# Kernel optimization log

Hardware: AMD Instinct MI355X
Metric: run time of the kernel (lower is better)

## Reference

```python
import jax, jax.numpy as jnp
import numpy as np

SIGMA = 1.0   # noise std (unit-variance synthetic input)
P = 11        # patch size p1
K = 16        # number of similar patches k1
WIN = 65      # search window w (odd)
S = 3         # reference-patch stride
ALPHA = 0.5   # n2n alpha


def _unfold(x, ksize, stride):
    # (N,1,H,W) -> (N, ksize*ksize, Ho, Wo); kernel positions row-major (== torch F.unfold for C=1)
    return jax.lax.conv_general_dilated_patches(
        x, (ksize, ksize), (stride, stride), 'VALID',
        dimension_numbers=('NCHW', 'OIHW', 'NCHW'))


def block_matching(x, k, p, w, s):
    N, _, H, W = x.shape
    v = w // 2
    assert (H - p + 1) % s == 1 and (W - p + 1) % s == 1  # no edge-case branches needed
    Href = (H - p) // s + 1
    Wref = (W - p) // s + 1
    x_pad = jnp.pad(x, ((0, 0), (0, 0), (v, v), (v, v)))  # zero pad; invalid candidates masked below
    # |patch|^2 / p^2 at every position of the padded image (== F.avg_pool2d(x**2, p))
    sq = jax.lax.reduce_window(x_pad * x_pad, 0.0, jax.lax.add,
                               (1, 1, p, p), (1, 1, 1, 1), 'VALID') / (p * p)
    norms = _unfold(sq, 2 * v + 1, s)                                  # (N,(2v+1)^2,Href,Wref)
    norms = norms.reshape(N, 2 * v + 1, 2 * v + 1, Href, Wref).transpose(0, 3, 4, 1, 2)
    lw = _unfold(x_pad, 2 * v + p, s) / p                              # (N,(2v+p)^2,Href,Wref)
    lw = lw.reshape(N, 2 * v + p, 2 * v + p, Href, Wref).transpose(0, 3, 4, 1, 2)
    G = N * Href * Wref
    lw = lw.reshape(1, G, 2 * v + p, 2 * v + p)
    ref = lw[0, :, v:-v, v:-v][:, None]                                # (G,1,p,p) reference patches
    sp = jax.lax.conv_general_dilated(
        lw, ref, (1, 1), 'VALID',
        dimension_numbers=('NCHW', 'OIHW', 'NCHW'),
        feature_group_count=G)                                         # (1,G,2v+1,2v+1)
    dist = norms.reshape(1, G, 2 * v + 1, 2 * v + 1) - 2.0 * sp
    dist = dist.reshape(N, Href, Wref, 2 * v + 1, 2 * v + 1)
    # mask candidate patches that fall outside the original image (torch uses NaN padding + topk)
    offs = jnp.arange(-v, v + 1)
    hr = jnp.arange(Href) * s
    wr = jnp.arange(Wref) * s
    row_ok = (hr[:, None] + offs >= 0) & (hr[:, None] + offs <= H - p)  # (Href, 2v+1)
    col_ok = (wr[:, None] + offs >= 0) & (wr[:, None] + offs <= W - p)  # (Wref, 2v+1)
    valid = row_ok[:, None, :, None] & col_ok[None, :, None, :]
    dist = jnp.where(valid[None], dist, jnp.inf)
    dist = dist.at[..., v, v].set(-jnp.inf)                            # reference patch always kept
    dist = dist.reshape(N, Href, Wref, (2 * v + 1) ** 2)
    _, idx = jax.lax.top_k(-dist, k)                                   # k smallest distances
    ind_row = idx // (2 * v + 1) - v
    ind_col = idx % (2 * v + 1) - v
    ind = (ind_row + hr[None, :, None, None]) * (W - p + 1) + (ind_col + wr[None, None, :, None])
    return ind.reshape(N, -1)                                          # (N, Href*Wref*k)


def gather_groups(y, indices, k, p):
    N = y.shape[0]
    uf = _unfold(y, p, 1).reshape(N, p * p, -1)                        # (N, n, (H-p+1)(W-p+1))
    Yg = jnp.take_along_axis(uf, indices[:, None, :], axis=2)          # (N, n, L*k)
    L = indices.shape[1] // k
    return Yg.reshape(N, p * p, L, k).transpose(0, 2, 3, 1)            # (N, L, k, n)


def denoise1(Y, sigma):
    # method='n2n', constraints='affine'
    N, B, k, n = Y.shape
    D = n * sigma ** 2
    E = n * ALPHA ** 2 * sigma ** 2
    Ik = jnp.eye(k, dtype=Y.dtype)
    Q = Y @ jnp.swapaxes(Y, 2, 3) + E * Ik                             # (N,B,k,k), SPD
    Lc = jnp.linalg.cholesky(Q)
    Ikb = jnp.broadcast_to(Ik, Q.shape)
    Z = jax.scipy.linalg.solve_triangular(Lc, Ikb, lower=True)
    Qinv = jax.scipy.linalg.solve_triangular(jnp.swapaxes(Lc, 2, 3), Z, lower=False)
    Qinv1 = jnp.sum(Qinv, axis=3, keepdims=True)
    Qinv2 = jnp.sum(Qinv1, axis=2, keepdims=True)
    theta = Ik - (Qinv - (Qinv1 @ jnp.swapaxes(Qinv1, 2, 3)) / Qinv2) * (D + E)
    theta = jnp.swapaxes(theta, 2, 3)
    X_hat = theta @ Y
    weights = 1.0 / jnp.clip(jnp.sum(theta * theta, axis=3, keepdims=True), 1.0 / k, 1.0)
    return X_hat, weights


def _fold(x, H, W, p):
    # inverse of unfold: sum overlapping p x p patches back onto the image grid
    N, n, _ = x.shape
    Hp, Wp = H - p + 1, W - p + 1
    x = x.reshape(N, p, p, Hp, Wp)
    out = jnp.zeros((N, 1, H, W), x.dtype)
    for a in range(p):
        for b in range(p):
            out = out.at[:, 0, a:a + Hp, b:b + Wp].add(x[:, a, b])
    return out


def aggregate(X_hat, weights, indices, H, W, p):
    N, L, k, n = X_hat.shape
    X = (X_hat * weights).reshape(N, L * k, n).transpose(0, 2, 1)      # (N, n, L*k)
    Wt = jnp.broadcast_to(weights, (N, L, k, n)).reshape(N, L * k, n).transpose(0, 2, 1)
    Lfull = (H - p + 1) * (W - p + 1)
    def scat(vals, idx):
        return jnp.zeros((n, Lfull), vals.dtype).at[:, idx].add(vals)
    X_sum = jax.vmap(scat)(X, indices)
    W_sum = jax.vmap(scat)(Wt, indices)
    return _fold(X_sum, H, W, p) / _fold(W_sum, H, W, p)


def _forward(y):
    N, C, H, W = y.shape
    indices = block_matching(y, K, P, WIN, S)
    Yg = gather_groups(y, indices, K, P)
    X_hat, weights = denoise1(Yg, SIGMA)
    return aggregate(X_hat, weights, indices, H, W, P)


def setup_inputs():
    key = jax.random.key(0)
    y = jax.random.normal(key, (4, 1, 128, 128), dtype=jnp.float32)
    return {"y": y}


def reference(y):
    return _forward(y)
```

## Files before the change

### kernel.cpp

```cpp
#include <hip/hip_runtime.h>
#include <math.h>

#define HH 128
#define WW 128
#define NIMG 4
#define PP 11
#define KSIM 16
#define STRIDE_S 3
#define VRAD 32
#define WINW 65
#define NTASK (WINW*9)
#define HREF 40
#define WREF 40
#define NPOS 118
#define WROWS 75
#define WPITCH 84
#define NGROUP (NIMG*HREF*WREF)
#define EPS_E 30.25f
#define DE_C 151.25f
#define INFD 3.0e38f
#define RTASK 292
#define THREC 152

__global__ __launch_bounds__(256, 5)
void bm_kernel(const float* __restrict__ y, int* __restrict__ inds)
{
    __shared__ float win[WROWS][WPITCH];
    __shared__ float swv[4];
    __shared__ int   swi[4];

    const int blk = blockIdx.x;
    const int n   = blk / (HREF*WREF);
    const int rem = blk % (HREF*WREF);
    const int hr  = (rem / WREF) * STRIDE_S;
    const int wr  = (rem % WREF) * STRIDE_S;
    const float* img = y + n * HH * WW;
    const int tid = threadIdx.x;

    for (int t = tid; t < WROWS * WPITCH; t += 256) {
        int r = t / WPITCH, c = t % WPITCH;
        int gr = hr - VRAD + r, gc = wr - VRAD + c;
        float v = 0.f;
        if (c < WROWS && gr >= 0 && gr < HH && gc >= 0 && gc < WW)
            v = img[gr * WW + gc];
        win[r][c] = v;
    }
    __syncthreads();

    float d[3][8];
#pragma unroll
    for (int s = 0; s < 3; s++)
#pragma unroll
        for (int c = 0; c < 8; c++) d[s][c] = INFD;

#pragma unroll
    for (int s = 0; s < 3; s++) {
        int task = tid + (s << 8);
        if (task < NTASK) {
            int drx = task % WINW;
            int c0  = (task / WINW) * 8;
            int rr  = hr + drx - VRAD;
            bool rowok = (rr >= 0 && rr <= HH - PP);
            if (rowok) {
                float dot[8];
                float colsq[18];
#pragma unroll
                for (int c = 0; c < 8; c++) dot[c] = 0.f;
#pragma unroll
                for (int j2 = 0; j2 < 18; j2++) colsq[j2] = 0.f;
                for (int a = 0; a < PP; a++) {
                    const float4* w4 = reinterpret_cast<const float4*>(&win[drx + a][c0]);
                    float4 A0 = w4[0], A1 = w4[1], A2 = w4[2], A3 = w4[3];
                    float2 A4 = *reinterpret_cast<const float2*>(&win[drx + a][c0 + 16]);
                    float wv[18] = {A0.x,A0.y,A0.z,A0.w, A1.x,A1.y,A1.z,A1.w,
                                    A2.x,A2.y,A2.z,A2.w, A3.x,A3.y,A3.z,A3.w,
                                    A4.x,A4.y};
                    const float4* r4 = reinterpret_cast<const float4*>(&win[VRAD + a][VRAD]);
                    float4 R0 = r4[0], R1 = r4[1];
                    float2 R2 = *reinterpret_cast<const float2*>(&win[VRAD + a][VRAD + 8]);
                    float  R3 = win[VRAD + a][VRAD + 10];
                    float rv[11] = {R0.x,R0.y,R0.z,R0.w, R1.x,R1.y,R1.z,R1.w,
                                    R2.x,R2.y, R3};
#pragma unroll
                    for (int j2 = 0; j2 < 18; j2++) colsq[j2] += wv[j2] * wv[j2];
#pragma unroll
                    for (int b = 0; b < PP; b++) {
#pragma unroll
                        for (int c = 0; c < 8; c++)
                            dot[c] += wv[b + c] * rv[b];
                    }
                }
#pragma unroll
                for (int j2 = 1; j2 < 18; j2++) colsq[j2] += colsq[j2 - 1];
#pragma unroll
                for (int c = 0; c < 8; c++) {
                    int dcx = c0 + c;
                    int cc  = wr + dcx - VRAD;
                    float norm = colsq[c + 10] - (c ? colsq[c - 1] : 0.f);
                    if (dcx < WINW && cc >= 0 && cc <= WW - PP)
                        d[s][c] = norm - 2.f * dot[c];
                }
            }
            if (task == RTASK) d[s][0] = -INFD;
        }
    }

    float lval = INFD; int lidx = 0;
#pragma unroll
    for (int s = 0; s < 3; s++)
#pragma unroll
        for (int c = 0; c < 8; c++)
            if (d[s][c] < lval) { lval = d[s][c]; lidx = (s << 3) | c; }

    for (int sel = 0; sel < KSIM; sel++) {
        float rv = lval;
        int   ri = ((tid + ((lidx >> 3) << 8)) << 3) | (lidx & 7);
#pragma unroll
        for (int off = 32; off > 0; off >>= 1) {
            float ov = __shfl_down(rv, off);
            int   oi = __shfl_down(ri, off);
            if (ov < rv) { rv = ov; ri = oi; }
        }
        if ((tid & 63) == 0) { swv[tid >> 6] = rv; swi[tid >> 6] = ri; }
        __syncthreads();
        float bval = swv[0]; int bidx = swi[0];
#pragma unroll
        for (int w2 = 1; w2 < 4; w2++)
            if (swv[w2] < bval) { bval = swv[w2]; bidx = swi[w2]; }
        if (tid == 0) {
            int task2 = bidx >> 3;
            int drx = task2 % WINW;
            int dcx = (task2 / WINW) * 8 + (bidx & 7);
            inds[blk * KSIM + sel] =
                (hr + drx - VRAD) * NPOS + (wr + dcx - VRAD);
        }
        __syncthreads();
        int otid = (bidx >> 3) & 255;
        if (tid == otid) {
            int code = (((bidx >> 3) >> 8) << 3) | (bidx & 7);
            lval = INFD; lidx = 0;
#pragma unroll
            for (int s = 0; s < 3; s++)
#pragma unroll
                for (int c = 0; c < 8; c++) {
                    if (((s << 3) | c) == code) d[s][c] = INFD;
                    if (d[s][c] < lval) { lval = d[s][c]; lidx = (s << 3) | c; }
                }
        }
    }
}

__global__ __launch_bounds__(256)
void dn_solve(const float* __restrict__ y, const int* __restrict__ inds,
              float* __restrict__ thW)
{
    __shared__ float Yp[4][16][124];
    __shared__ float Qs[4][16][17];
    __shared__ float s1[4][16];
    __shared__ float s2[4];
    __shared__ float wl[4][16];
    __shared__ short pr_[4][16], pc_[4][16];

    const int blk = blockIdx.x;
    const int tid = threadIdx.x;
    const int g0 = blk * 4;

    if (tid < 64) {
        int gq = tid >> 4, m = tid & 15;
        int idx = inds[(g0 + gq) * KSIM + m];
        pr_[gq][m] = (short)(idx / NPOS);
        pc_[gq][m] = (short)(idx % NPOS);
    }
    if (tid < 192) {
        int gq = tid / 48, m = (tid / 3) % 16, e = tid % 3;
        Yp[gq][m][121 + e] = 0.f;
    }
    __syncthreads();

    for (int t = tid; t < 4 * 16 * 121; t += 256) {
        int gq = t / 1936, m = (t / 121) % 16, j = t % 121;
        int a = j / PP, b = j % PP;
        const float* img = y + ((g0 + gq) / (HREF * WREF)) * HH * WW;
        Yp[gq][m][j] = img[((int)pr_[gq][m] + a) * WW + (int)pc_[gq][m] + b];
    }
    __syncthreads();

    for (int t = tid; t < 4 * 136; t += 256) {
        int gq = t / 136, e = t % 136;
        int i = (int)((sqrtf(8.f * (float)e + 1.f) - 1.f) * 0.5f + 1e-4f);
        int j = e - i * (i + 1) / 2;
        const float4* Yi = reinterpret_cast<const float4*>(&Yp[gq][i][0]);
        const float4* Yj = reinterpret_cast<const float4*>(&Yp[gq][j][0]);
        float s = (i == j) ? EPS_E : 0.f;
#pragma unroll
        for (int q = 0; q < 31; q++) {
            float4 xi = Yi[q], xj = Yj[q];
            s += xi.x * xj.x; s += xi.y * xj.y;
            s += xi.z * xj.z; s += xi.w * xj.w;
        }
        Qs[gq][i][j] = s;
        Qs[gq][j][i] = s;
    }
    __syncthreads();

    const int gq = tid >> 6, ii = (tid >> 2) & 15, jq = tid & 3;
    for (int ks = 0; ks < 16; ks++) {
        float fA = Qs[gq][ii][ks];
        float pv = Qs[gq][ks][ks];
        float rk[4], aij[4];
#pragma unroll
        for (int q = 0; q < 4; q++) {
            rk[q]  = Qs[gq][ks][jq * 4 + q];
            aij[q] = Qs[gq][ii][jq * 4 + q];
        }
        __syncthreads();
        float inv = 1.f / pv;
#pragma unroll
        for (int q = 0; q < 4; q++) {
            int jj = jq * 4 + q;
            float nv;
            if (ii == ks) nv = (jj == ks) ? inv : rk[q] * inv;
            else          nv = (jj == ks) ? -fA * inv : aij[q] - fA * rk[q] * inv;
            Qs[gq][ii][jj] = nv;
        }
        __syncthreads();
    }

    if (jq == 0) {
        float s = 0.f;
#pragma unroll
        for (int b = 0; b < 16; b++) s += Qs[gq][ii][b];
        s1[gq][ii] = s;
    }
    __syncthreads();
    if (ii == 0 && jq == 0) {
        float s = 0.f;
#pragma unroll
        for (int a = 0; a < 16; a++) s += s1[gq][a];
        s2[gq] = s;
    }
    __syncthreads();
    {
        float s1i = s1[gq][ii];
#pragma unroll
        for (int q = 0; q < 4; q++) {
            int jj = jq * 4 + q;
            float t2 = ((ii == jj) ? 1.f : 0.f)
                     - (Qs[gq][ii][jj] - s1i * s1[gq][jj] / s2[gq]) * DE_C;
            Qs[gq][ii][jj] = t2;
        }
    }
    __syncthreads();
    if (jq == 1) {
        float s = 0.f;
#pragma unroll
        for (int m = 0; m < 16; m++) { float t2 = Qs[gq][m][ii]; s += t2 * t2; }
        s = fminf(fmaxf(s, 1.f / 16.f), 1.f);
        wl[gq][ii] = 1.f / s;
    }
    __syncthreads();

    for (int t = tid; t < 4 * THREC; t += 256) {
        int gg = t / THREC, e = t % THREC;
        float v;
        if (e < 136) {
            int i = (int)((sqrtf(8.f * (float)e + 1.f) - 1.f) * 0.5f + 1e-4f);
            int j = e - i * (i + 1) / 2;
            v = Qs[gg][i][j];
        } else {
            v = wl[gg][e - 136];
        }
        thW[(size_t)(g0 + gg) * THREC + e] = v;
    }
}

__global__ __launch_bounds__(512)
void dn_scatter(const float* __restrict__ y, const int* __restrict__ inds,
                const float* __restrict__ thW, float2* __restrict__ nd, int R)
{
    __shared__ float2 acc[84][85];
    __shared__ float  Athw[16][16][16];
    __shared__ float  wlS[16][16];
    __shared__ int    pOff[16][16];
    __shared__ int    pBase[16][16];

    const int blk = blockIdx.x;
    const int n  = blk / 100;
    const int tr = blk % 100;
    const int ti = tr / 10, tj = tr % 10;
    const int r0 = 12 * ti - VRAD, c0 = 12 * tj - VRAD;
    const int tid = threadIdx.x;
    const float* img = y + n * HH * WW;

    if (tid < 256) {
        int g = tid >> 4, m = tid & 15;
        int gg = n * (HREF * WREF) + (ti * 4 + (g >> 2)) * WREF + (tj * 4 + (g & 3));
        int idx = inds[gg * KSIM + m];
        int pr = idx / NPOS, pc = idx % NPOS;
        pOff[g][m]  = (pr - r0) * 85 + (pc - c0);
        pBase[g][m] = pr * WW + pc;
        wlS[g][m]   = thW[(size_t)gg * THREC + 136 + m];
    }
    __syncthreads();
    for (int t = tid; t < 16 * 256; t += 512) {
        int g = t >> 8, m = (t >> 4) & 15, r = t & 15;
        int gg = n * (HREF * WREF) + (ti * 4 + (g >> 2)) * WREF + (tj * 4 + (g & 3));
        int hi = (m > r) ? m : r, lo = (m > r) ? r : m;
        Athw[g][m][r] = thW[(size_t)gg * THREC + hi * (hi + 1) / 2 + lo] * wlS[g][r];
    }
    for (int t = tid; t < 84 * 85; t += 512)
        ((float2*)acc)[t] = make_float2(0.f, 0.f);
    __syncthreads();

    for (int it = 0; it < 4; it++) {
        int task = tid + it * 512;
        if (task < 16 * 121) {
            int g = task / 121, px = task % 121;
            int dra = px / PP, dca = px % PP;
            const int off  = dra * WW + dca;
            const int offA = dra * 85 + dca;
            float xw[16];
#pragma unroll
            for (int r = 0; r < 16; r++) xw[r] = 0.f;
#pragma unroll
            for (int m = 0; m < 16; m++) {
                float yv = img[pBase[g][m] + off];
                const float4* Arow = reinterpret_cast<const float4*>(&Athw[g][m][0]);
                float4 A0 = Arow[0], A1 = Arow[1], A2 = Arow[2], A3 = Arow[3];
                xw[0]  += A0.x * yv; xw[1]  += A0.y * yv;
                xw[2]  += A0.z * yv; xw[3]  += A0.w * yv;
                xw[4]  += A1.x * yv; xw[5]  += A1.y * yv;
                xw[6]  += A1.z * yv; xw[7]  += A1.w * yv;
                xw[8]  += A2.x * yv; xw[9]  += A2.y * yv;
                xw[10] += A2.z * yv; xw[11] += A2.w * yv;
                xw[12] += A3.x * yv; xw[13] += A3.y * yv;
                xw[14] += A3.z * yv; xw[15] += A3.w * yv;
            }
#pragma unroll
            for (int r = 0; r < 16; r++) {
                float* cell = (float*)acc + 2 * (pOff[g][r] + offA);
                __hip_atomic_fetch_add(cell,     xw[r],
                    __ATOMIC_RELAXED, __HIP_MEMORY_SCOPE_WORKGROUP);
                __hip_atomic_fetch_add(cell + 1, wlS[g][r],
                    __ATOMIC_RELAXED, __HIP_MEMORY_SCOPE_WORKGROUP);
            }
        }
    }
    __syncthreads();

    float2* ndI = nd + ((size_t)(blk & (R - 1)) * NIMG + n) * HH * WW;
    for (int t = tid; t < 84 * 84; t += 512) {
        int rr = t / 84, cc = t % 84;
        float2 vv = acc[rr][cc];
        if (vv.y != 0.f) {
            int px = (r0 + rr) * WW + (c0 + cc);
#if defined(__has_builtin) && __has_builtin(__builtin_amdgcn_global_atomic_fadd_v2f32)
            typedef float v2f __attribute__((ext_vector_type(2)));
            __builtin_amdgcn_global_atomic_fadd_v2f32((v2f*)&ndI[px], (v2f){vv.x, vv.y});
#else
            atomicAdd(&ndI[px].x, vv.x);
            atomicAdd(&ndI[px].y, vv.y);
#endif
        }
    }
}

__global__ __launch_bounds__(256)
void fin_kernel(const float2* __restrict__ nd, float* __restrict__ out, int R)
{
    int t = blockIdx.x * 256 + threadIdx.x;
    if (t < NIMG * HH * WW) {
        float sn = 0.f, sd = 0.f;
        for (int r = 0; r < R; r++) {
            float2 vv = nd[(size_t)r * NIMG * HH * WW + t];
            sn += vv.x; sd += vv.y;
        }
        out[t] = sn / sd;
    }
}

extern "C" void kernel_launch(void* const* d_in, const int* in_sizes, int n_in,
                              void* d_out, int out_size, void* d_ws, size_t ws_size,
                              hipStream_t stream)
{
    const float* y = (const float*)d_in[0];
    float* out = (float*)d_out;

    size_t perRep = (size_t)NIMG * HH * WW * sizeof(float2);
    size_t indsB  = (size_t)NGROUP * KSIM * sizeof(int);
    size_t thWB   = (size_t)NGROUP * THREC * sizeof(float);
    int R = 1;
    while (R < 4 && perRep * (size_t)(R * 2) + indsB + thWB <= ws_size) R <<= 1;

    float2* nd   = (float2*)d_ws;
    int*    inds = (int*)((char*)d_ws + perRep * (size_t)R);
    float*  thW  = (float*)((char*)inds + indsB);

    hipMemsetAsync(nd, 0, perRep * (size_t)R, stream);
    bm_kernel<<<NGROUP, 256, 0, stream>>>(y, inds);
    dn_solve<<<NGROUP / 4, 256, 0, stream>>>(y, inds, thW);
    dn_scatter<<<NIMG * 100, 512, 0, stream>>>(y, inds, thW, nd, R);
    fin_kernel<<<(NIMG * HH * WW + 255) / 256, 256, 0, stream>>>(nd, out, R);
}
```

Baseline: 427.8 us.

## Split scatter tiles in half and process two pixels per thread

The scatter kernel now launches twice as many blocks, each covering half of a 4x4 group tile (8 groups) with a smaller shared accumulator of 78 rows. Each thread computes two adjacent patch pixels, so every Athw row it loads from shared memory is reused for both. The block-matching kernel's occupancy hint is raised from 5 to 6. The aim is more parallelism and less shared-memory traffic, at the cost of more overlapping halo flushes to global atomics and higher register pressure.

```diff
diff --git a/kernel.cpp b/kernel.cpp
--- a/kernel.cpp
+++ b/kernel.cpp
@@ -22,7 +22,7 @@
 #define RTASK 292
 #define THREC 152
 
-__global__ __launch_bounds__(256, 5)
+__global__ __launch_bounds__(256, 6)
 void bm_kernel(const float* __restrict__ y, int* __restrict__ inds)
 {
     __shared__ float win[WROWS][WPITCH];
@@ -274,27 +274,31 @@
     }
 }
 
-__global__ __launch_bounds__(512)
+__global__ __launch_bounds__(512, 1)
 void dn_scatter(const float* __restrict__ y, const int* __restrict__ inds,
                 const float* __restrict__ thW, float2* __restrict__ nd, int R)
 {
-    __shared__ float2 acc[84][85];
-    __shared__ float  Athw[16][16][16];
-    __shared__ float  wlS[16][16];
-    __shared__ int    pOff[16][16];
-    __shared__ int    pBase[16][16];
+    __shared__ float2 acc[78][85];
+    __shared__ float  Athw[8][16][16];
+    __shared__ float  wlS[8][16];
+    __shared__ int    pOff[8][16];
+    __shared__ int    pBase[8][16];
 
     const int blk = blockIdx.x;
-    const int n  = blk / 100;
-    const int tr = blk % 100;
+    const int n   = blk / 200;
+    const int rem = blk % 200;
+    const int tr  = rem >> 1;
+    const int hf  = rem & 1;
     const int ti = tr / 10, tj = tr % 10;
-    const int r0 = 12 * ti - VRAD, c0 = 12 * tj - VRAD;
+    const int r0 = 12 * ti + 6 * hf - VRAD;
+    const int c0 = 12 * tj - VRAD;
     const int tid = threadIdx.x;
     const float* img = y + n * HH * WW;
 
-    if (tid < 256) {
+    if (tid < 128) {
         int g = tid >> 4, m = tid & 15;
-        int gg = n * (HREF * WREF) + (ti * 4 + (g >> 2)) * WREF + (tj * 4 + (g & 3));
+        int u = 2 * hf + (g >> 2), v = g & 3;
+        int gg = n * (HREF * WREF) + (ti * 4 + u) * WREF + (tj * 4 + v);
         int idx = inds[gg * KSIM + m];
         int pr = idx / NPOS, pc = idx % NPOS;
         pOff[g][m]  = (pr - r0) * 85 + (pc - c0);
@@ -302,46 +306,66 @@
         wlS[g][m]   = thW[(size_t)gg * THREC + 136 + m];
     }
     __syncthreads();
-    for (int t = tid; t < 16 * 256; t += 512) {
+    for (int t = tid; t < 8 * 256; t += 512) {
         int g = t >> 8, m = (t >> 4) & 15, r = t & 15;
-        int gg = n * (HREF * WREF) + (ti * 4 + (g >> 2)) * WREF + (tj * 4 + (g & 3));
+        int u = 2 * hf + (g >> 2), v = g & 3;
+        int gg = n * (HREF * WREF) + (ti * 4 + u) * WREF + (tj * 4 + v);
         int hi = (m > r) ? m : r, lo = (m > r) ? r : m;
         Athw[g][m][r] = thW[(size_t)gg * THREC + hi * (hi + 1) / 2 + lo] * wlS[g][r];
     }
-    for (int t = tid; t < 84 * 85; t += 512)
+    for (int t = tid; t < 78 * 85; t += 512)
         ((float2*)acc)[t] = make_float2(0.f, 0.f);
     __syncthreads();
 
-    for (int it = 0; it < 4; it++) {
-        int task = tid + it * 512;
-        if (task < 16 * 121) {
-            int g = task / 121, px = task % 121;
-            int dra = px / PP, dca = px % PP;
-            const int off  = dra * WW + dca;
-            const int offA = dra * 85 + dca;
-            float xw[16];
-#pragma unroll
-            for (int r = 0; r < 16; r++) xw[r] = 0.f;
-#pragma unroll
-            for (int m = 0; m < 16; m++) {
-                float yv = img[pBase[g][m] + off];
-                const float4* Arow = reinterpret_cast<const float4*>(&Athw[g][m][0]);
-                float4 A0 = Arow[0], A1 = Arow[1], A2 = Arow[2], A3 = Arow[3];
-                xw[0]  += A0.x * yv; xw[1]  += A0.y * yv;
-                xw[2]  += A0.z * yv; xw[3]  += A0.w * yv;
-                xw[4]  += A1.x * yv; xw[5]  += A1.y * yv;
-                xw[6]  += A1.z * yv; xw[7]  += A1.w * yv;
-                xw[8]  += A2.x * yv; xw[9]  += A2.y * yv;
-                xw[10] += A2.z * yv; xw[11] += A2.w * yv;
-                xw[12] += A3.x * yv; xw[13] += A3.y * yv;
-                xw[14] += A3.z * yv; xw[15] += A3.w * yv;
-            }
-#pragma unroll
-            for (int r = 0; r < 16; r++) {
-                float* cell = (float*)acc + 2 * (pOff[g][r] + offA);
-                __hip_atomic_fetch_add(cell,     xw[r],
+    if (tid < 8 * 61) {
+        int g = tid / 61, s = tid % 61;
+        int pxa = 2 * s;
+        bool okB = (pxa + 1 < 121);
+        int dra = pxa / PP, dca = pxa % PP;
+        int drb = dra, dcb = dca + 1;
+        if (dcb == PP) { drb = dra + 1; dcb = 0; }
+        if (!okB) { drb = dra; dcb = dca; }
+        const int offA  = dra * WW + dca,  offB  = drb * WW + dcb;
+        const int offA8 = dra * 85 + dca,  offB8 = drb * 85 + dcb;
+        float xwA[16], xwB[16];
+#pragma unroll
+        for (int r = 0; r < 16; r++) { xwA[r] = 0.f; xwB[r] = 0.f; }
+#pragma unroll
+        for (int m = 0; m < 16; m++) {
+            float yvA = img[pBase[g][m] + offA];
+            float yvB = img[pBase[g][m] + offB];
+            const float4* Arow = reinterpret_cast<const float4*>(&Athw[g][m][0]);
+            float4 A0 = Arow[0], A1 = Arow[1], A2 = Arow[2], A3 = Arow[3];
+            xwA[0]  += A0.x * yvA; xwB[0]  += A0.x * yvB;
+            xwA[1]  += A0.y * yvA; xwB[1]  += A0.y * yvB;
+            xwA[2]  += A0.z * yvA; xwB[2]  += A0.z * yvB;
+            xwA[3]  += A0.w * yvA; xwB[3]  += A0.w * yvB;
+            xwA[4]  += A1.x * yvA; xwB[4]  += A1.x * yvB;
+            xwA[5]  += A1.y * yvA; xwB[5]  += A1.y * yvB;
+            xwA[6]  += A1.z * yvA; xwB[6]  += A1.z * yvB;
+            xwA[7]  += A1.w * yvA; xwB[7]  += A1.w * yvB;
+            xwA[8]  += A2.x * yvA; xwB[8]  += A2.x * yvB;
+            xwA[9]  += A2.y * yvA; xwB[9]  += A2.y * yvB;
+            xwA[10] += A2.z * yvA; xwB[10] += A2.z * yvB;
+            xwA[11] += A2.w * yvA; xwB[11] += A2.w * yvB;
+            xwA[12] += A3.x * yvA; xwB[12] += A3.x * yvB;
+            xwA[13] += A3.y * yvA; xwB[13] += A3.y * yvB;
+            xwA[14] += A3.z * yvA; xwB[14] += A3.z * yvB;
+            xwA[15] += A3.w * yvA; xwB[15] += A3.w * yvB;
+        }
+#pragma unroll
+        for (int r = 0; r < 16; r++) {
+            float w = wlS[g][r];
+            float* cA = (float*)acc + 2 * (pOff[g][r] + offA8);
+            __hip_atomic_fetch_add(cA,     xwA[r],
+                __ATOMIC_RELAXED, __HIP_MEMORY_SCOPE_WORKGROUP);
+            __hip_atomic_fetch_add(cA + 1, w,
+                __ATOMIC_RELAXED, __HIP_MEMORY_SCOPE_WORKGROUP);
+            if (okB) {
+                float* cB = (float*)acc + 2 * (pOff[g][r] + offB8);
+                __hip_atomic_fetch_add(cB,     xwB[r],
                     __ATOMIC_RELAXED, __HIP_MEMORY_SCOPE_WORKGROUP);
-                __hip_atomic_fetch_add(cell + 1, wlS[g][r],
+                __hip_atomic_fetch_add(cB + 1, w,
                     __ATOMIC_RELAXED, __HIP_MEMORY_SCOPE_WORKGROUP);
             }
         }
@@ -349,7 +373,7 @@
     __syncthreads();
 
     float2* ndI = nd + ((size_t)(blk & (R - 1)) * NIMG + n) * HH * WW;
-    for (int t = tid; t < 84 * 84; t += 512) {
+    for (int t = tid; t < 78 * 84; t += 512) {
         int rr = t / 84, cc = t % 84;
         float2 vv = acc[rr][cc];
         if (vv.y != 0.f) {
@@ -399,6 +423,6 @@
     hipMemsetAsync(nd, 0, perRep * (size_t)R, stream);
     bm_kernel<<<NGROUP, 256, 0, stream>>>(y, inds);
     dn_solve<<<NGROUP / 4, 256, 0, stream>>>(y, inds, thW);
-    dn_scatter<<<NIMG * 100, 512, 0, stream>>>(y, inds, thW, nd, R);
+    dn_scatter<<<NIMG * 200, 512, 0, stream>>>(y, inds, thW, nd, R);
     fin_kernel<<<(NIMG * HH * WW + 255) / 256, 256, 0, stream>>>(nd, out, R);
 }
```

After: 470.2 us. 1.1x slower.

## Fuse per-group Gram solve into block-matching kernel using shared search window

Applied to the files above, without the earlier changes.

Folds the dn_solve kernel into the end of bm_kernel. The selected patch positions are kept in shared memory, and the 16x16 Gram matrix is built straight from the already-loaded search window instead of re-gathering patches from global memory. The Gauss-Jordan inverse, weight computation and thW store then run once per block. This removes a kernel launch and the global re-read of indices and patches, but adds shared memory and serial tail work to bm_kernel, which may reduce its occupancy (launch bounds request 5 blocks per CU).

```diff
diff --git a/kernel.cpp b/kernel.cpp
--- a/kernel.cpp
+++ b/kernel.cpp
@@ -23,11 +23,17 @@
 #define THREC 152
 
 __global__ __launch_bounds__(256, 5)
-void bm_kernel(const float* __restrict__ y, int* __restrict__ inds)
+void bm_kernel(const float* __restrict__ y, int* __restrict__ inds,
+               float* __restrict__ thW)
 {
     __shared__ float win[WROWS][WPITCH];
     __shared__ float swv[4];
     __shared__ int   swi[4];
+    __shared__ short selr[16], selc[16];
+    __shared__ float Qs[16][17];
+    __shared__ float s1v[16];
+    __shared__ float s2v;
+    __shared__ float wlv[16];
 
     const int blk = blockIdx.x;
     const int n   = blk / (HREF*WREF);
@@ -131,8 +137,10 @@
             int task2 = bidx >> 3;
             int drx = task2 % WINW;
             int dcx = (task2 / WINW) * 8 + (bidx & 7);
-            inds[blk * KSIM + sel] =
-                (hr + drx - VRAD) * NPOS + (wr + dcx - VRAD);
+            int prr = hr + drx - VRAD, pcc = wr + dcx - VRAD;
+            inds[blk * KSIM + sel] = prr * NPOS + pcc;
+            selr[sel] = (short)prr;
+            selc[sel] = (short)pcc;
         }
         __syncthreads();
         int otid = (bidx >> 3) & 255;
@@ -148,129 +156,86 @@
                 }
         }
     }
-}
-
-__global__ __launch_bounds__(256)
-void dn_solve(const float* __restrict__ y, const int* __restrict__ inds,
-              float* __restrict__ thW)
-{
-    __shared__ float Yp[4][16][124];
-    __shared__ float Qs[4][16][17];
-    __shared__ float s1[4][16];
-    __shared__ float s2[4];
-    __shared__ float wl[4][16];
-    __shared__ short pr_[4][16], pc_[4][16];
-
-    const int blk = blockIdx.x;
-    const int tid = threadIdx.x;
-    const int g0 = blk * 4;
-
-    if (tid < 64) {
-        int gq = tid >> 4, m = tid & 15;
-        int idx = inds[(g0 + gq) * KSIM + m];
-        pr_[gq][m] = (short)(idx / NPOS);
-        pc_[gq][m] = (short)(idx % NPOS);
-    }
-    if (tid < 192) {
-        int gq = tid / 48, m = (tid / 3) % 16, e = tid % 3;
-        Yp[gq][m][121 + e] = 0.f;
-    }
-    __syncthreads();
-
-    for (int t = tid; t < 4 * 16 * 121; t += 256) {
-        int gq = t / 1936, m = (t / 121) % 16, j = t % 121;
-        int a = j / PP, b = j % PP;
-        const float* img = y + ((g0 + gq) / (HREF * WREF)) * HH * WW;
-        Yp[gq][m][j] = img[((int)pr_[gq][m] + a) * WW + (int)pc_[gq][m] + b];
-    }
-    __syncthreads();
-
-    for (int t = tid; t < 4 * 136; t += 256) {
-        int gq = t / 136, e = t % 136;
+    __syncthreads();
+
+    if (tid < 136) {
+        int e = tid;
         int i = (int)((sqrtf(8.f * (float)e + 1.f) - 1.f) * 0.5f + 1e-4f);
         int j = e - i * (i + 1) / 2;
-        const float4* Yi = reinterpret_cast<const float4*>(&Yp[gq][i][0]);
-        const float4* Yj = reinterpret_cast<const float4*>(&Yp[gq][j][0]);
+        int ri0 = (int)selr[i] - hr + VRAD, ci0 = (int)selc[i] - wr + VRAD;
+        int rj0 = (int)selr[j] - hr + VRAD, cj0 = (int)selc[j] - wr + VRAD;
         float s = (i == j) ? EPS_E : 0.f;
-#pragma unroll
-        for (int q = 0; q < 31; q++) {
-            float4 xi = Yi[q], xj = Yj[q];
-            s += xi.x * xj.x; s += xi.y * xj.y;
-            s += xi.z * xj.z; s += xi.w * xj.w;
-        }
-        Qs[gq][i][j] = s;
-        Qs[gq][j][i] = s;
-    }
-    __syncthreads();
-
-    const int gq = tid >> 6, ii = (tid >> 2) & 15, jq = tid & 3;
+        for (int a = 0; a < PP; a++) {
+            const float* Ri = &win[ri0 + a][ci0];
+            const float* Rj = &win[rj0 + a][cj0];
+#pragma unroll
+            for (int b = 0; b < PP; b++) s += Ri[b] * Rj[b];
+        }
+        Qs[i][j] = s;
+        Qs[j][i] = s;
+    }
+    __syncthreads();
+
+    const int ii = tid >> 4, jj = tid & 15;
     for (int ks = 0; ks < 16; ks++) {
-        float fA = Qs[gq][ii][ks];
-        float pv = Qs[gq][ks][ks];
-        float rk[4], aij[4];
-#pragma unroll
-        for (int q = 0; q < 4; q++) {
-            rk[q]  = Qs[gq][ks][jq * 4 + q];
-            aij[q] = Qs[gq][ii][jq * 4 + q];
-        }
-        __syncthreads();
-        float inv = 1.f / pv;
-#pragma unroll
-        for (int q = 0; q < 4; q++) {
-            int jj = jq * 4 + q;
+        float fA = 0.f, rk = 0.f, pv = 1.f, aij = 0.f;
+        if (tid < 256) {
+            fA  = Qs[ii][ks];
+            rk  = Qs[ks][jj];
+            pv  = Qs[ks][ks];
+            aij = Qs[ii][jj];
+        }
+        __syncthreads();
+        if (tid < 256) {
+            float inv = 1.f / pv;
             float nv;
-            if (ii == ks) nv = (jj == ks) ? inv : rk[q] * inv;
-            else          nv = (jj == ks) ? -fA * inv : aij[q] - fA * rk[q] * inv;
-            Qs[gq][ii][jj] = nv;
-        }
-        __syncthreads();
-    }
-
-    if (jq == 0) {
+            if (ii == ks) nv = (jj == ks) ? inv : rk * inv;
+            else          nv = (jj == ks) ? -fA * inv : aij - fA * rk * inv;
+            Qs[ii][jj] = nv;
+        }
+        __syncthreads();
+    }
+
+    if (tid < 16) {
         float s = 0.f;
 #pragma unroll
-        for (int b = 0; b < 16; b++) s += Qs[gq][ii][b];
-        s1[gq][ii] = s;
-    }
-    __syncthreads();
-    if (ii == 0 && jq == 0) {
+        for (int b = 0; b < 16; b++) s += Qs[tid][b];
+        s1v[tid] = s;
+    }
+    __syncthreads();
+    if (tid == 0) {
         float s = 0.f;
 #pragma unroll
-        for (int a = 0; a < 16; a++) s += s1[gq][a];
-        s2[gq] = s;
+        for (int a = 0; a < 16; a++) s += s1v[a];
+        s2v = s;
     }
     __syncthreads();
     {
-        float s1i = s1[gq][ii];
-#pragma unroll
-        for (int q = 0; q < 4; q++) {
-            int jj = jq * 4 + q;
-            float t2 = ((ii == jj) ? 1.f : 0.f)
-                     - (Qs[gq][ii][jj] - s1i * s1[gq][jj] / s2[gq]) * DE_C;
-            Qs[gq][ii][jj] = t2;
-        }
-    }
-    __syncthreads();
-    if (jq == 1) {
+        float t2 = ((ii == jj) ? 1.f : 0.f)
+                 - (Qs[ii][jj] - s1v[ii] * s1v[jj] / s2v) * DE_C;
+        __syncthreads();
+        Qs[ii][jj] = t2;
+    }
+    __syncthreads();
+    if (tid < 16) {
         float s = 0.f;
 #pragma unroll
-        for (int m = 0; m < 16; m++) { float t2 = Qs[gq][m][ii]; s += t2 * t2; }
+        for (int m = 0; m < 16; m++) { float t2 = Qs[m][tid]; s += t2 * t2; }
         s = fminf(fmaxf(s, 1.f / 16.f), 1.f);
-        wl[gq][ii] = 1.f / s;
-    }
-    __syncthreads();
-
-    for (int t = tid; t < 4 * THREC; t += 256) {
-        int gg = t / THREC, e = t % THREC;
+        wlv[tid] = 1.f / s;
+    }
+    __syncthreads();
+
+    if (tid < THREC) {
         float v;
-        if (e < 136) {
-            int i = (int)((sqrtf(8.f * (float)e + 1.f) - 1.f) * 0.5f + 1e-4f);
-            int j = e - i * (i + 1) / 2;
-            v = Qs[gg][i][j];
+        if (tid < 136) {
+            int i = (int)((sqrtf(8.f * (float)tid + 1.f) - 1.f) * 0.5f + 1e-4f);
+            int j = tid - i * (i + 1) / 2;
+            v = Qs[i][j];
         } else {
-            v = wl[gg][e - 136];
-        }
-        thW[(size_t)(g0 + gg) * THREC + e] = v;
+            v = wlv[tid - 136];
+        }
+        thW[(size_t)blk * THREC + tid] = v;
     }
 }
 
@@ -397,8 +362,7 @@
     float*  thW  = (float*)((char*)inds + indsB);
 
     hipMemsetAsync(nd, 0, perRep * (size_t)R, stream);
-    bm_kernel<<<NGROUP, 256, 0, stream>>>(y, inds);
-    dn_solve<<<NGROUP / 4, 256, 0, stream>>>(y, inds, thW);
+    bm_kernel<<<NGROUP, 256, 0, stream>>>(y, inds, thW);
     dn_scatter<<<NIMG * 100, 512, 0, stream>>>(y, inds, thW, nd, R);
     fin_kernel<<<(NIMG * HH * WW + 255) / 256, 256, 0, stream>>>(nd, out, R);
 }
```

Result: no change. 435.8 us (+1.9%).
